# Optimization experiments

Measured on AMD Instinct MI355X. Metric: run time of the kernel, lower is better.

## Reference

```python
import jax, jax.numpy as jnp
import numpy as np

MUL = 16            # multiplicity of 0e and 1o in irreps_in/irreps_out
N_NODES = 12500
N_EDGES = 200000
EDGE_ATTR_DIM = 16
WEIGHT_NUMEL = 4 * MUL * MUL  # 4 uvw paths, mul_sh = 1


def setup_inputs() -> dict:
    key = jax.random.key(0)
    ks = jax.random.split(key, 8)
    node_attr = jax.random.normal(ks[0], (N_NODES, 4 * MUL), dtype=jnp.float32)
    edge_index = jax.random.randint(ks[1], (2, N_EDGES), 0, N_NODES, dtype=jnp.int64)
    edge_attr = jax.random.normal(ks[2], (N_EDGES, EDGE_ATTR_DIM), dtype=jnp.float32)
    edge_sh = jax.random.normal(ks[3], (N_EDGES, 4), dtype=jnp.float32)
    # radial ScalarMLP params: Linear(16,16) + SiLU + Linear(16, weight_numel)
    s1 = 1.0 / np.sqrt(EDGE_ATTR_DIM)
    w1 = jax.random.uniform(ks[4], (EDGE_ATTR_DIM, EDGE_ATTR_DIM), jnp.float32, -s1, s1)
    b1 = jax.random.uniform(ks[5], (EDGE_ATTR_DIM,), jnp.float32, -s1, s1)
    w2 = jax.random.uniform(ks[6], (EDGE_ATTR_DIM, WEIGHT_NUMEL), jnp.float32, -s1, s1)
    b2 = jax.random.uniform(ks[7], (WEIGHT_NUMEL,), jnp.float32, -s1, s1)
    return {"node_attr": node_attr, "edge_index": edge_index, "edge_attr": edge_attr,
            "edge_sh": edge_sh, "w1": w1, "b1": b1, "w2": w2, "b2": b2}


def _conv(node_attr, edge_index, edge_attr, edge_sh, w1, b1, w2, b2):
    N = node_attr.shape[0]
    E = edge_attr.shape[0]
    src, dst = edge_index[0], edge_index[1]

    # gather source node features per edge
    x = node_attr[src]                         # [E, 4*MUL]
    x0 = x[:, :MUL]                            # [E, MUL]    (16x0e)
    x1 = x[:, MUL:].reshape(E, MUL, 3)         # [E, MUL, 3] (16x1o)
    y0 = edge_sh[:, 0]                         # [E]   (1x0e)
    y1 = edge_sh[:, 1:4]                       # [E,3] (1x1o)

    # radial MLP -> per-edge tensor-product weights
    h = jax.nn.silu(edge_attr @ w1 + b1)
    W = (h @ w2 + b2).reshape(E, 4, MUL, MUL)  # 4 uvw paths, [E,4,u,w]

    alpha = 1.0 / np.sqrt(2 * MUL).astype(np.float32)  # path norm: 2 paths * MUL fan-in per out irrep
    inv_sqrt3 = np.float32(1.0 / np.sqrt(3.0))

    # path 0: 0e x 0e -> 0e (CG = 1)
    out0 = jnp.einsum('eu,euw->ew', x0 * y0[:, None], W[:, 0])
    # path 1: 1o x 1o -> 0e (CG = delta_ij / sqrt(3), component-normalized)
    out0 = out0 + inv_sqrt3 * jnp.einsum('eui,ei,euw->ew', x1, y1, W[:, 1])
    # path 2: 0e x 1o -> 1o (CG = identity)
    out1 = jnp.einsum('eu,ei,euw->ewi', x0, y1, W[:, 2])
    # path 3: 1o x 0e -> 1o (CG = identity)
    out1 = out1 + jnp.einsum('eui,e,euw->ewi', x1, y0, W[:, 3])

    out_ij = jnp.concatenate([alpha * out0, (alpha * out1).reshape(E, 3 * MUL)], axis=-1)

    # scatter-mean into destination nodes
    sums = jax.ops.segment_sum(out_ij, dst, num_segments=N)
    counts = jax.ops.segment_sum(jnp.ones((E,), out_ij.dtype), dst, num_segments=N)
    return sums / jnp.maximum(counts, 1.0)[:, None]


def reference(node_attr, edge_index, edge_attr, edge_sh, w1, b1, w2, b2):
    return _conv(node_attr, edge_index, edge_attr, edge_sh, w1, b1, w2, b2)
```

## Files before the change

### kernel.cpp

```cpp
#include <hip/hip_runtime.h>
#include <math.h>

#define E_TOTAL  200000
#define NNODES   12500
#define OUT_ELEM 800000
#define NTILE    (E_TOTAL / 64)
#define PAD      64

typedef float    f32x4 __attribute__((ext_vector_type(4)));
typedef _Float16 f16x8 __attribute__((ext_vector_type(8)));
typedef _Float16 f16x4 __attribute__((ext_vector_type(4)));
typedef _Float16 f16x2 __attribute__((ext_vector_type(2)));

union AF { f16x8 f; f16x2 h2[4]; };

static const size_t OFF_CNT    = (size_t)NNODES * PAD * 64 * 2;
static const size_t OFF_BFRAG  = (OFF_CNT + (size_t)NNODES * 4 + 15) & ~(size_t)15;
static const size_t WS_NEEDED  = OFF_BFRAG + (size_t)36 * 64 * 8 * 2;

__global__ void k_prep(const float* __restrict__ w2, const float* __restrict__ b2,
                       int* __restrict__ cnt, _Float16* __restrict__ bfrag) {
    const int g = blockIdx.x * 256 + threadIdx.x;
    if (g < NNODES) cnt[g] = 0;
    if (g < 36 * 64) {
        const int slot = g >> 6, lane = g & 63;
        const int br = slot / 9, kb = slot - br * 9;
        const int quad = lane >> 4, n = lane & 15;
        const float alpha = 0.17677669529663687f;
        _Float16* dst = bfrag + (size_t)g * 8;
        #pragma unroll
        for (int j = 0; j < 8; ++j) {
            float v;
            if (kb < 8) {
                const int ku = kb * 32 + quad * 8 + j;
                v = w2[(ku >> 4) * 1024 + br * 256 + (ku & 15) * 16 + n];
            } else {
                const int loc = quad * 8 + j;
                v = (loc < 16) ? b2[br * 256 + loc * 16 + n] : 0.0f;
            }
            dst[j] = (_Float16)(alpha * v);
        }
    }
}

__global__ __launch_bounds__(256) void k_conv(
        const float* __restrict__ node_attr,
        const int*   __restrict__ edge_index,
        const float* __restrict__ edge_attr,
        const float* __restrict__ edge_sh,
        const float* __restrict__ w1,
        const float* __restrict__ b1,
        const f16x8* __restrict__ bfrag,
        int* __restrict__ cnt,
        _Float16* __restrict__ edge_pad)
{
    const int t = threadIdx.x;
    __shared__ float  sh_h[64][17];
    __shared__ float4 sh_y[64];
    __shared__ _Float16 sh_s[6][64][24];
    __shared__ int    sh_row[64];

    const int ebase = blockIdx.x * 64;
    const float inv_sqrt3 = 0.57735026918962576f;

    if (t < 64) {
        const int e2 = ebase + t;
        const int d = edge_index[E_TOTAL + e2];
        int slot = atomicAdd(&cnt[d], 1);
        if (slot >= PAD) slot = PAD - 1;
        sh_row[t] = d * PAD + slot;
    }

    {
        const int e_loc = t & 63, kq = t >> 6;
        const int e = ebase + e_loc;
        const float* ea = edge_attr + (size_t)e * 16;
        float ear[16];
        #pragma unroll
        for (int dq = 0; dq < 4; ++dq) {
            float4 v = *(const float4*)(ea + dq * 4);
            ear[dq * 4 + 0] = v.x; ear[dq * 4 + 1] = v.y;
            ear[dq * 4 + 2] = v.z; ear[dq * 4 + 3] = v.w;
        }
        float4 acc = *(const float4*)(b1 + kq * 4);
        #pragma unroll
        for (int d = 0; d < 16; ++d) {
            float4 wr = *(const float4*)(w1 + d * 16 + kq * 4);
            acc.x += ear[d] * wr.x; acc.y += ear[d] * wr.y;
            acc.z += ear[d] * wr.z; acc.w += ear[d] * wr.w;
        }
        sh_h[e_loc][kq * 4 + 0] = acc.x / (1.0f + __expf(-acc.x));
        sh_h[e_loc][kq * 4 + 1] = acc.y / (1.0f + __expf(-acc.y));
        sh_h[e_loc][kq * 4 + 2] = acc.z / (1.0f + __expf(-acc.z));
        sh_h[e_loc][kq * 4 + 3] = acc.w / (1.0f + __expf(-acc.w));
    }

    {
        const int e_loc = (t & 15) + ((t >> 6) << 4);
        const int pp = (t >> 4) & 3;
        const int u0 = pp * 4;
        const int e = ebase + e_loc;
        const int src = edge_index[e];
        const float4 yv = *(const float4*)(edge_sh + (size_t)e * 4);
        const float* xp = node_attr + (size_t)src * 64;
        float4 x0v = *(const float4*)(xp + u0);
        float x1v[4][3];
        #pragma unroll
        for (int q = 0; q < 4; ++q)
            #pragma unroll
            for (int i = 0; i < 3; ++i)
                x1v[q][i] = xp[16 + (u0 + q) * 3 + i];
        const float* x0p = &x0v.x;
        f16x4 s0h, s1h, x0h, ah, bh, ch;
        #pragma unroll
        for (int q = 0; q < 4; ++q) {
            s0h[q] = (_Float16)(x0p[q] * yv.x);
            s1h[q] = (_Float16)(inv_sqrt3 * (x1v[q][0] * yv.y + x1v[q][1] * yv.z + x1v[q][2] * yv.w));
            x0h[q] = (_Float16)x0p[q];
            ah[q]  = (_Float16)x1v[q][0];
            bh[q]  = (_Float16)x1v[q][1];
            ch[q]  = (_Float16)x1v[q][2];
        }
        *(f16x4*)&sh_s[0][e_loc][u0] = s0h;
        *(f16x4*)&sh_s[1][e_loc][u0] = s1h;
        *(f16x4*)&sh_s[2][e_loc][u0] = x0h;
        *(f16x4*)&sh_s[3][e_loc][u0] = ah;
        *(f16x4*)&sh_s[4][e_loc][u0] = bh;
        *(f16x4*)&sh_s[5][e_loc][u0] = ch;
        if (pp == 0) sh_y[e_loc] = yv;
    }
    __syncthreads();

    const int lane = t & 63, wv = t >> 6;
    const int m = lane & 15, quad = lane >> 4;
    const int e_loc = wv * 16 + m;
    const int qh = quad >> 1, ql = quad & 1;

    AF svh[6];
    #pragma unroll
    for (int b = 0; b < 6; ++b)
        svh[b].f = *(const f16x8*)&sh_s[b][e_loc][ql * 8];
    float hreg[8];
    #pragma unroll
    for (int kb = 0; kb < 8; ++kb) hreg[kb] = sh_h[e_loc][2 * kb + qh];

    f32x4 acc0  = {0.f, 0.f, 0.f, 0.f};
    f32x4 acc2  = {0.f, 0.f, 0.f, 0.f};
    f32x4 acc3a = {0.f, 0.f, 0.f, 0.f};
    f32x4 acc3b = {0.f, 0.f, 0.f, 0.f};
    f32x4 acc3c = {0.f, 0.f, 0.f, 0.f};

    for (int kb = 0; kb < 9; ++kb) {
        const f16x8 B0 = bfrag[(0 * 9 + kb) * 64 + lane];
        const f16x8 B1 = bfrag[(1 * 9 + kb) * 64 + lane];
        const f16x8 B2 = bfrag[(2 * 9 + kb) * 64 + lane];
        const f16x8 B3 = bfrag[(3 * 9 + kb) * 64 + lane];
        const float selF = (kb < 8) ? hreg[kb] : ((quad < 2) ? 1.0f : 0.0f);
        const _Float16 sh1 = (_Float16)selF;
        const f16x2 sel2 = (f16x2){sh1, sh1};
        AF A[6];
        #pragma unroll
        for (int b = 0; b < 6; ++b)
            #pragma unroll
            for (int p = 0; p < 4; ++p)
                A[b].h2[p] = sel2 * svh[b].h2[p];
        acc0  = __builtin_amdgcn_mfma_f32_16x16x32_f16(A[0].f, B0, acc0, 0, 0, 0);
        acc0  = __builtin_amdgcn_mfma_f32_16x16x32_f16(A[1].f, B1, acc0, 0, 0, 0);
        acc2  = __builtin_amdgcn_mfma_f32_16x16x32_f16(A[2].f, B2, acc2, 0, 0, 0);
        acc3a = __builtin_amdgcn_mfma_f32_16x16x32_f16(A[3].f, B3, acc3a, 0, 0, 0);
        acc3b = __builtin_amdgcn_mfma_f32_16x16x32_f16(A[4].f, B3, acc3b, 0, 0, 0);
        acc3c = __builtin_amdgcn_mfma_f32_16x16x32_f16(A[5].f, B3, acc3c, 0, 0, 0);
    }

    #pragma unroll
    for (int r = 0; r < 4; ++r) {
        const int el = wv * 16 + quad * 4 + r;
        const float4 yv = sh_y[el];
        const float t2v = acc2[r];
        const float o0 = acc0[r];
        const float oa = yv.y * t2v + yv.x * acc3a[r];
        const float ob = yv.z * t2v + yv.x * acc3b[r];
        const float oc = yv.w * t2v + yv.x * acc3c[r];
        f16x4 pk = {(_Float16)o0, (_Float16)oa, (_Float16)ob, (_Float16)oc};
        const int row = sh_row[el];
        *(f16x4*)(edge_pad + (size_t)row * 64 + m * 4) = pk;
    }
}

__global__ __launch_bounds__(256) void k_gather(const _Float16* __restrict__ edge_pad,
                                                const int* __restrict__ cnt,
                                                float* __restrict__ out) {
    const int t = threadIdx.x;
    const int lane = t & 63;
    const int n = blockIdx.x * 4 + (t >> 6);
    int pe;
    if (lane < 16) pe = lane * 4;
    else { const int idx = lane - 16; const int w = idx / 3; pe = w * 4 + 1 + (idx - w * 3); }
    int c = cnt[n];
    if (c > PAD) c = PAD;
    const _Float16* base = edge_pad + (size_t)n * PAD * 64 + pe;
    float a0 = 0.0f, a1 = 0.0f;
    int j = 0;
    for (; j + 2 <= c; j += 2) {
        a0 += (float)base[(size_t)j * 64];
        a1 += (float)base[(size_t)(j + 1) * 64];
    }
    if (j < c) a0 += (float)base[(size_t)j * 64];
    const float acc = a0 + a1;
    out[n * 64 + lane] = acc / (c > 0 ? (float)c : 1.0f);
}

__global__ void k_zero_f(float* __restrict__ out, float* __restrict__ counts) {
    int i = blockIdx.x * 256 + threadIdx.x;
    if (i < OUT_ELEM) out[i] = 0.0f;
    if (i < NNODES)   counts[i] = 0.0f;
}

#define EPB 80
#define NE  8
__global__ __launch_bounds__(256) void k_conv_atomic(
        const float* __restrict__ node_attr,
        const int*   __restrict__ edge_index,
        const float* __restrict__ edge_attr,
        const float* __restrict__ edge_sh,
        const float* __restrict__ w1,
        const float* __restrict__ b1,
        const float* __restrict__ w2,
        const float* __restrict__ b2,
        float* __restrict__ out,
        float* __restrict__ counts)
{
    const int thr   = threadIdx.x;
    const int lane  = thr & 63;
    const int wv    = thr >> 6;
    const int u     = lane >> 2;
    const int wbase = (lane & 3) * 4;

    float4 w2r[16];
    #pragma unroll
    for (int k = 0; k < 16; ++k)
        w2r[k] = *(const float4*)(w2 + k * 1024 + thr * 4);
    const float4 b2r = *(const float4*)(b2 + thr * 4);

    __shared__ __align__(16) float sh_h[NE][16];
    __shared__ float sh_s0[NE][16];
    __shared__ float sh_s1[NE][16];
    __shared__ float sh_x0[NE][16];
    __shared__ float sh_x1[NE][16][3];
    __shared__ float sh_y0[NE];
    __shared__ float sh_y1[NE][3];
    __shared__ int   sh_dst[NE];

    const float alpha     = 0.17677669529663687f;
    const float inv_sqrt3 = 0.57735026918962576f;
    const int e0 = blockIdx.x * EPB;

    for (int batch = 0; batch < EPB / NE; ++batch) {
        const int ebase = e0 + batch * NE;
        if (thr < 128) {
            const int le = thr >> 4, k = thr & 15;
            const int e = ebase + le;
            float acc = b1[k];
            const float* ea = edge_attr + (size_t)e * 16;
            #pragma unroll
            for (int d = 0; d < 16; ++d) acc += ea[d] * w1[d * 16 + k];
            sh_h[le][k] = acc / (1.0f + __expf(-acc));
            if (k == 0) sh_dst[le] = edge_index[E_TOTAL + e];
        } else {
            const int le = (thr - 128) >> 4, uu = thr & 15;
            const int e = ebase + le;
            const int src = edge_index[e];
            const float y0  = edge_sh[e * 4 + 0];
            const float y1a = edge_sh[e * 4 + 1];
            const float y1b = edge_sh[e * 4 + 2];
            const float y1c = edge_sh[e * 4 + 3];
            const float* xp = node_attr + (size_t)src * 64;
            const float x0v = xp[uu];
            const float xa = xp[16 + uu * 3 + 0];
            const float xb = xp[16 + uu * 3 + 1];
            const float xc = xp[16 + uu * 3 + 2];
            sh_x0[le][uu] = x0v;
            sh_x1[le][uu][0] = xa; sh_x1[le][uu][1] = xb; sh_x1[le][uu][2] = xc;
            sh_s0[le][uu] = x0v * y0;
            sh_s1[le][uu] = inv_sqrt3 * (xa * y1a + xb * y1b + xc * y1c);
            if (uu == 0) {
                sh_y0[le] = y0;
                sh_y1[le][0] = y1a; sh_y1[le][1] = y1b; sh_y1[le][2] = y1c;
            }
        }
        __syncthreads();

        for (int le = 0; le < NE; ++le) {
            float W0 = b2r.x, W1 = b2r.y, W2c = b2r.z, W3c = b2r.w;
            const float4* hv = (const float4*)sh_h[le];
            #pragma unroll
            for (int kk = 0; kk < 4; ++kk) {
                const float4 h4 = hv[kk];
                const int kb = kk * 4;
                W0  += h4.x * w2r[kb + 0].x; W1  += h4.x * w2r[kb + 0].y;
                W2c += h4.x * w2r[kb + 0].z; W3c += h4.x * w2r[kb + 0].w;
                W0  += h4.y * w2r[kb + 1].x; W1  += h4.y * w2r[kb + 1].y;
                W2c += h4.y * w2r[kb + 1].z; W3c += h4.y * w2r[kb + 1].w;
                W0  += h4.z * w2r[kb + 2].x; W1  += h4.z * w2r[kb + 2].y;
                W2c += h4.z * w2r[kb + 2].z; W3c += h4.z * w2r[kb + 2].w;
                W0  += h4.w * w2r[kb + 3].x; W1  += h4.w * w2r[kb + 3].y;
                W2c += h4.w * w2r[kb + 3].z; W3c += h4.w * w2r[kb + 3].w;
            }
            const int dst = sh_dst[le];
            float* op = out + (size_t)dst * 64;
            if (wv == 0 || wv == 1) {
                const float s = (wv == 0) ? sh_s0[le][u] : sh_s1[le][u];
                float v0 = s * W0, v1 = s * W1, v2 = s * W2c, v3 = s * W3c;
                #pragma unroll
                for (int off = 4; off <= 32; off <<= 1) {
                    v0 += __shfl_xor(v0, off); v1 += __shfl_xor(v1, off);
                    v2 += __shfl_xor(v2, off); v3 += __shfl_xor(v3, off);
                }
                if (lane < 4) {
                    atomicAdd(op + wbase + 0, alpha * v0);
                    atomicAdd(op + wbase + 1, alpha * v1);
                    atomicAdd(op + wbase + 2, alpha * v2);
                    atomicAdd(op + wbase + 3, alpha * v3);
                    if (wv == 0 && lane == 0) atomicAdd(&counts[dst], 1.0f);
                }
            } else if (wv == 2) {
                const float s = sh_x0[le][u];
                float v0 = s * W0, v1 = s * W1, v2 = s * W2c, v3 = s * W3c;
                #pragma unroll
                for (int off = 4; off <= 32; off <<= 1) {
                    v0 += __shfl_xor(v0, off); v1 += __shfl_xor(v1, off);
                    v2 += __shfl_xor(v2, off); v3 += __shfl_xor(v3, off);
                }
                if (lane < 4) {
                    const float ya = alpha * sh_y1[le][0];
                    const float yb = alpha * sh_y1[le][1];
                    const float yc = alpha * sh_y1[le][2];
                    float vv[4] = {v0, v1, v2, v3};
                    #pragma unroll
                    for (int q = 0; q < 4; ++q) {
                        float* qp = op + 16 + (wbase + q) * 3;
                        atomicAdd(qp + 0, vv[q] * ya);
                        atomicAdd(qp + 1, vv[q] * yb);
                        atomicAdd(qp + 2, vv[q] * yc);
                    }
                }
            } else {
                const float ay0 = alpha * sh_y0[le];
                #pragma unroll
                for (int i = 0; i < 3; ++i) {
                    const float s = sh_x1[le][u][i];
                    float v0 = s * W0, v1 = s * W1, v2 = s * W2c, v3 = s * W3c;
                    #pragma unroll
                    for (int off = 4; off <= 32; off <<= 1) {
                        v0 += __shfl_xor(v0, off); v1 += __shfl_xor(v1, off);
                        v2 += __shfl_xor(v2, off); v3 += __shfl_xor(v3, off);
                    }
                    if (lane < 4) {
                        atomicAdd(op + 16 + (wbase + 0) * 3 + i, ay0 * v0);
                        atomicAdd(op + 16 + (wbase + 1) * 3 + i, ay0 * v1);
                        atomicAdd(op + 16 + (wbase + 2) * 3 + i, ay0 * v2);
                        atomicAdd(op + 16 + (wbase + 3) * 3 + i, ay0 * v3);
                    }
                }
            }
        }
        __syncthreads();
    }
}

__global__ void k_div(float* __restrict__ out, const float* __restrict__ counts) {
    int i = blockIdx.x * 256 + threadIdx.x;
    if (i < OUT_ELEM) {
        float c = counts[i >> 6];
        out[i] *= 1.0f / fmaxf(c, 1.0f);
    }
}

extern "C" void kernel_launch(void* const* d_in, const int* in_sizes, int n_in,
                              void* d_out, int out_size, void* d_ws, size_t ws_size,
                              hipStream_t stream) {
    const float* node_attr  = (const float*)d_in[0];
    const int*   edge_index = (const int*)d_in[1];
    const float* edge_attr  = (const float*)d_in[2];
    const float* edge_sh    = (const float*)d_in[3];
    const float* w1         = (const float*)d_in[4];
    const float* b1         = (const float*)d_in[5];
    const float* w2         = (const float*)d_in[6];
    const float* b2         = (const float*)d_in[7];
    float* out = (float*)d_out;

    if (ws_size >= WS_NEEDED) {
        char* ws = (char*)d_ws;
        _Float16* edge_pad = (_Float16*)ws;
        int*      cnt      = (int*)(ws + OFF_CNT);
        _Float16* bfrag    = (_Float16*)(ws + OFF_BFRAG);

        k_prep<<<(NNODES + 255) / 256, 256, 0, stream>>>(w2, b2, cnt, bfrag);
        k_conv<<<NTILE, 256, 0, stream>>>(
            node_attr, edge_index, edge_attr, edge_sh, w1, b1,
            (const f16x8*)bfrag, cnt, edge_pad);
        k_gather<<<NNODES / 4, 256, 0, stream>>>(edge_pad, cnt, out);
    } else {
        float* counts = (float*)d_ws;
        k_zero_f<<<(OUT_ELEM + 255) / 256, 256, 0, stream>>>(out, counts);
        k_conv_atomic<<<E_TOTAL / EPB, 256, 0, stream>>>(
            node_attr, edge_index, edge_attr, edge_sh, w1, b1, w2, b2, out, counts);
        k_div<<<(OUT_ELEM + 255) / 256, 256, 0, stream>>>(out, counts);
    }
}
```

Before: 137.0 us.

## Write edge outputs contiguously and gather via per-node edge index lists

The conv kernel now writes each edge's fp16 output row at its own edge index, so stores are contiguous, instead of scattering rows into a padded per-node slot buffer. It records the edge id in a per-node position table. The gather kernel loads the position list into lanes, broadcasts each id with a shuffle, and reads the edge rows indirectly with four accumulators. This shrinks the workspace and aims to make the conv stores more coalesced, at the cost of indirect, less sequential reads and an extra position-table load in the gather.

```diff
diff --git a/kernel.cpp b/kernel.cpp
--- a/kernel.cpp
+++ b/kernel.cpp
@@ -14,8 +14,9 @@
 
 union AF { f16x8 f; f16x2 h2[4]; };
 
-static const size_t OFF_CNT    = (size_t)NNODES * PAD * 64 * 2;
-static const size_t OFF_BFRAG  = (OFF_CNT + (size_t)NNODES * 4 + 15) & ~(size_t)15;
+static const size_t OFF_CNT    = (size_t)E_TOTAL * 64 * 2;
+static const size_t OFF_POS    = OFF_CNT + (size_t)NNODES * 4;
+static const size_t OFF_BFRAG  = (OFF_POS + (size_t)NNODES * PAD * 4 + 15) & ~(size_t)15;
 static const size_t WS_NEEDED  = OFF_BFRAG + (size_t)36 * 64 * 8 * 2;
 
 __global__ void k_prep(const float* __restrict__ w2, const float* __restrict__ b2,
@@ -52,13 +53,13 @@
         const float* __restrict__ b1,
         const f16x8* __restrict__ bfrag,
         int* __restrict__ cnt,
-        _Float16* __restrict__ edge_pad)
+        int* __restrict__ pos,
+        _Float16* __restrict__ edge_out)
 {
     const int t = threadIdx.x;
     __shared__ float  sh_h[64][17];
     __shared__ float4 sh_y[64];
     __shared__ _Float16 sh_s[6][64][24];
-    __shared__ int    sh_row[64];
 
     const int ebase = blockIdx.x * 64;
     const float inv_sqrt3 = 0.57735026918962576f;
@@ -68,7 +69,7 @@
         const int d = edge_index[E_TOTAL + e2];
         int slot = atomicAdd(&cnt[d], 1);
         if (slot >= PAD) slot = PAD - 1;
-        sh_row[t] = d * PAD + slot;
+        pos[d * PAD + slot] = e2;
     }
 
     {
@@ -182,13 +183,13 @@
         const float ob = yv.z * t2v + yv.x * acc3b[r];
         const float oc = yv.w * t2v + yv.x * acc3c[r];
         f16x4 pk = {(_Float16)o0, (_Float16)oa, (_Float16)ob, (_Float16)oc};
-        const int row = sh_row[el];
-        *(f16x4*)(edge_pad + (size_t)row * 64 + m * 4) = pk;
-    }
-}
-
-__global__ __launch_bounds__(256) void k_gather(const _Float16* __restrict__ edge_pad,
+        *(f16x4*)(edge_out + (size_t)(ebase + el) * 64 + m * 4) = pk;
+    }
+}
+
+__global__ __launch_bounds__(256) void k_gather(const _Float16* __restrict__ edge_out,
                                                 const int* __restrict__ cnt,
+                                                const int* __restrict__ pos,
                                                 float* __restrict__ out) {
     const int t = threadIdx.x;
     const int lane = t & 63;
@@ -198,15 +199,24 @@
     else { const int idx = lane - 16; const int w = idx / 3; pe = w * 4 + 1 + (idx - w * 3); }
     int c = cnt[n];
     if (c > PAD) c = PAD;
-    const _Float16* base = edge_pad + (size_t)n * PAD * 64 + pe;
-    float a0 = 0.0f, a1 = 0.0f;
+    const int p = (lane < c) ? pos[n * PAD + lane] : 0;
+    float a0 = 0.f, a1 = 0.f, a2 = 0.f, a3 = 0.f;
     int j = 0;
-    for (; j + 2 <= c; j += 2) {
-        a0 += (float)base[(size_t)j * 64];
-        a1 += (float)base[(size_t)(j + 1) * 64];
-    }
-    if (j < c) a0 += (float)base[(size_t)j * 64];
-    const float acc = a0 + a1;
+    for (; j + 4 <= c; j += 4) {
+        const int r0 = __shfl(p, j + 0);
+        const int r1 = __shfl(p, j + 1);
+        const int r2 = __shfl(p, j + 2);
+        const int r3 = __shfl(p, j + 3);
+        a0 += (float)edge_out[(size_t)r0 * 64 + pe];
+        a1 += (float)edge_out[(size_t)r1 * 64 + pe];
+        a2 += (float)edge_out[(size_t)r2 * 64 + pe];
+        a3 += (float)edge_out[(size_t)r3 * 64 + pe];
+    }
+    for (; j < c; ++j) {
+        const int r = __shfl(p, j);
+        a0 += (float)edge_out[(size_t)r * 64 + pe];
+    }
+    const float acc = (a0 + a1) + (a2 + a3);
     out[n * 64 + lane] = acc / (c > 0 ? (float)c : 1.0f);
 }
 
@@ -391,15 +401,16 @@
 
     if (ws_size >= WS_NEEDED) {
         char* ws = (char*)d_ws;
-        _Float16* edge_pad = (_Float16*)ws;
+        _Float16* edge_out = (_Float16*)ws;
         int*      cnt      = (int*)(ws + OFF_CNT);
+        int*      pos      = (int*)(ws + OFF_POS);
         _Float16* bfrag    = (_Float16*)(ws + OFF_BFRAG);
 
         k_prep<<<(NNODES + 255) / 256, 256, 0, stream>>>(w2, b2, cnt, bfrag);
         k_conv<<<NTILE, 256, 0, stream>>>(
             node_attr, edge_index, edge_attr, edge_sh, w1, b1,
-            (const f16x8*)bfrag, cnt, edge_pad);
-        k_gather<<<NNODES / 4, 256, 0, stream>>>(edge_pad, cnt, out);
+            (const f16x8*)bfrag, cnt, pos, edge_out);
+        k_gather<<<NNODES / 4, 256, 0, stream>>>(edge_out, cnt, pos, out);
     } else {
         float* counts = (float*)d_ws;
         k_zero_f<<<(OUT_ELEM + 255) / 256, 256, 0, stream>>>(out, counts);
```

Result: faster. 124.2 us (median of 2 runs) (-9.3%).
